# Performance work log

Hardware: AMD Instinct MI355X
Metric: run time of the kernel (lower is better)

Reference implementation:

```python
import jax, jax.numpy as jnp
import numpy as np

TEMP = 0.1
W1, W2 = 0.5, 0.5
W3 = 1.0 - W1 - W2  # = 0.0, as in the original module defaults


def setup_inputs() -> dict:
    key = jax.random.key(0)
    ks = jax.random.split(key, 8)
    N, D = 131072, 256
    C1, C2, C3 = 1000, 100, 20
    features = jax.random.normal(ks[0], (N, D), dtype=jnp.float32) * 0.1
    prototypes_1 = jax.random.normal(ks[1], (C1, D), dtype=jnp.float32)
    labels_1 = jax.random.randint(ks[2], (N,), 0, C1)
    prototypes_2 = jax.random.normal(ks[3], (C2, D), dtype=jnp.float32)
    # ensure every coarse class appears (torch.unique == arange(C))
    labels_2 = jax.random.permutation(ks[4], jnp.arange(N) % C2)
    prototypes_3 = jax.random.normal(ks[5], (C3, D), dtype=jnp.float32)
    labels_3 = jax.random.permutation(ks[6], jnp.arange(N) % C3)
    return {
        "features": features,
        "prototypes_1": prototypes_1,
        "labels_1": labels_1,
        "prototypes_2": prototypes_2,
        "labels_2": labels_2,
        "prototypes_3": prototypes_3,
        "labels_3": labels_3,
    }


def _proto_nce(means, protos):
    # means: [C, D], protos: [C, D]; pos_mask(one_hot of unique=arange) is identity
    sim = (means @ protos.T) / TEMP              # [C, C]
    pos = jnp.diagonal(sim)                      # [C]
    return -jnp.mean(pos - jax.nn.logsumexp(sim, axis=1))


def _segment_mean(features, labels, num_segments):
    sums = jax.ops.segment_sum(features, labels, num_segments=num_segments)
    cnt = jax.ops.segment_sum(jnp.ones((labels.shape[0],), features.dtype),
                              labels, num_segments=num_segments)
    return sums / cnt[:, None]


def reference(features, prototypes_1, labels_1, prototypes_2, labels_2,
              prototypes_3, labels_3):
    # fine level: per-sample InfoNCE against fine prototypes
    fine_sim = (features @ prototypes_1.T) / TEMP            # [N, C1]
    fine_pos = jnp.take_along_axis(fine_sim, labels_1[:, None], axis=1)[:, 0]
    fine_loss = -jnp.mean(fine_pos - jax.nn.logsumexp(fine_sim, axis=1))

    # coarse level: per-class feature means (segment mean == masked-mean loop)
    coarse_means = _segment_mean(features, labels_2, prototypes_2.shape[0])
    coarse_loss = _proto_nce(coarse_means, prototypes_2)

    # con-coarse level
    con_means = _segment_mean(features, labels_3, prototypes_3.shape[0])
    con_coarse_loss = _proto_nce(con_means, prototypes_3)

    loss = W1 * fine_loss + W2 * coarse_loss + W3 * con_coarse_loss
    return (loss, fine_loss, coarse_loss, con_coarse_loss)
```

## Files before the change

kernel.cpp:

```cpp
#include <hip/hip_runtime.h>
#include <math.h>

#define WS_POS   0
#define WS_LSE   1
#define WS_ACC2  2
#define WS_ACC3  3
#define WS_S2    256
#define WS_S3    (256+25600)
#define WS_SEG   163840
#define NROWS    144
#define PART_FLOATS (NROWS*256 + 128)
#define PIMG_BYTE_OFF 131072

#define SC2  14.426950408889634f
#define BIAS 48.0f

typedef __attribute__((ext_vector_type(4))) float f32x4;
typedef __attribute__((ext_vector_type(8))) short short8;

static __device__ __forceinline__ unsigned f2bf(float f) {
    union { float f; unsigned u; } x; x.f = f;
    unsigned r = x.u + 0x7FFFu + ((x.u >> 16) & 1u);
    return r >> 16;
}

__global__ void k_zero(float* __restrict__ p, int count) {
    int i = blockIdx.x * 256 + threadIdx.x;
    if (i < count) p[i] = 0.f;
}

__global__ void k_prep(const float* __restrict__ p1, unsigned short* __restrict__ Pimg,
                       int C1) {
    int e = blockIdx.x * 256 + threadIdx.x;
    int r  = e >> 5;
    int k0 = (e & 31) * 8;
    unsigned h[8];
#pragma unroll
    for (int j = 0; j < 8; ++j)
        h[j] = (r < C1) ? f2bf(p1[(size_t)r * 256 + k0 + j]) : 0u;
    uint4 v;
    v.x = h[0] | (h[1] << 16);
    v.y = h[2] | (h[3] << 16);
    v.z = h[4] | (h[5] << 16);
    v.w = h[6] | (h[7] << 16);
    *(uint4*)(Pimg + (size_t)r * 256 + k0) = v;
}

__global__ __launch_bounds__(256, 2) void k_seg(
        const float* __restrict__ feat, const float* __restrict__ p1,
        const int* __restrict__ l1, const int* __restrict__ l2,
        const int* __restrict__ l3, float* __restrict__ ws,
        int partMask, int useAtomic) {
    __shared__ int labs23[512];
    __shared__ int labs1[512];
    __shared__ float psum[4];
    const int tid  = threadIdx.x;
    const int lane = tid & 63;
    const int wv   = tid >> 6;
    const int g    = lane >> 4;
    const int rs   = lane & 15;
    const int chunk = blockIdx.x >> 1, half = blockIdx.x & 1;
    const int base  = chunk * 512;
    const int dimbase = half * 128 + wv * 32;

    for (int j = tid; j < 512; j += 256) {
        labs23[j] = l2[base + j] | (l3[base + j] << 16);
        labs1[j]  = l1[base + j];
    }
    __syncthreads();

    f32x4 acc[9][2];
#pragma unroll
    for (int mt = 0; mt < 9; ++mt)
#pragma unroll
        for (int nt = 0; nt < 2; ++nt) acc[mt][nt] = (f32x4){0.f, 0.f, 0.f, 0.f};

    float fA[16], pA[16], fB[16], pB[16];
    float posacc = 0.f;

#define LOADSTEP(u, F, P) { \
    const int sl0 = (u) * 32 + 8 * g; \
    _Pragma("unroll") \
    for (int j = 0; j < 8; ++j) { \
        const int sl = sl0 + j; \
        const size_t fb = (size_t)(base + sl) * 256 + dimbase + rs; \
        F[j]     = feat[fb]; \
        F[8 + j] = feat[fb + 16]; \
        const size_t pb = (size_t)labs1[sl] * 256 + dimbase + rs; \
        P[j]     = p1[pb]; \
        P[8 + j] = p1[pb + 16]; \
    } }

#define PROCSTEP(u, F, P) { \
    _Pragma("unroll") \
    for (int j = 0; j < 16; ++j) posacc = fmaf(F[j], P[j], posacc); \
    union { unsigned w[4]; short8 s; } b0, b1; \
    _Pragma("unroll") \
    for (int q = 0; q < 4; ++q) { \
        asm("v_cvt_pk_bf16_f32 %0, %1, %2" : "=v"(b0.w[q]) : "v"(F[2*q]),   "v"(F[2*q+1])); \
        asm("v_cvt_pk_bf16_f32 %0, %1, %2" : "=v"(b1.w[q]) : "v"(F[8+2*q]), "v"(F[8+2*q+1])); \
    } \
    int d2[8], d3[8]; \
    { const int sl0 = (u) * 32 + 8 * g; \
      _Pragma("unroll") \
      for (int j = 0; j < 8; ++j) { \
          const int v = labs23[sl0 + j]; \
          d2[j] = (v & 0xffff) - rs; \
          d3[j] = (v >> 16) - rs; \
      } } \
    _Pragma("unroll") \
    for (int mt = 0; mt < 7; ++mt) { \
        union { unsigned w[4]; short8 s; } af; \
        _Pragma("unroll") \
        for (int q = 0; q < 4; ++q) { \
            unsigned w = (d2[2*q] == mt*16) ? 0x3F80u : 0u; \
            if (d2[2*q+1] == mt*16) w |= 0x3F800000u; \
            af.w[q] = w; \
        } \
        acc[mt][0] = __builtin_amdgcn_mfma_f32_16x16x32_bf16(af.s, b0.s, acc[mt][0], 0, 0, 0); \
        acc[mt][1] = __builtin_amdgcn_mfma_f32_16x16x32_bf16(af.s, b1.s, acc[mt][1], 0, 0, 0); \
    } \
    _Pragma("unroll") \
    for (int mt = 0; mt < 2; ++mt) { \
        union { unsigned w[4]; short8 s; } af; \
        _Pragma("unroll") \
        for (int q = 0; q < 4; ++q) { \
            unsigned w = (d3[2*q] == mt*16) ? 0x3F80u : 0u; \
            if (d3[2*q+1] == mt*16) w |= 0x3F800000u; \
            af.w[q] = w; \
        } \
        acc[7+mt][0] = __builtin_amdgcn_mfma_f32_16x16x32_bf16(af.s, b0.s, acc[7+mt][0], 0, 0, 0); \
        acc[7+mt][1] = __builtin_amdgcn_mfma_f32_16x16x32_bf16(af.s, b1.s, acc[7+mt][1], 0, 0, 0); \
    } }

    LOADSTEP(0, fA, pA);
#pragma unroll 1
    for (int t = 0; t < 16; t += 2) {
        LOADSTEP(t + 1, fB, pB);
        PROCSTEP(t, fA, pA);
        if (t + 2 < 16) LOADSTEP(t + 2, fA, pA);
        PROCSTEP(t + 1, fB, pB);
    }
#undef LOADSTEP
#undef PROCSTEP

    float* part = ws + WS_SEG +
        (size_t)(useAtomic ? (chunk & partMask) : chunk) * PART_FLOATS;
#pragma unroll
    for (int mt = 0; mt < 9; ++mt)
#pragma unroll
        for (int nt = 0; nt < 2; ++nt)
#pragma unroll
            for (int r = 0; r < 4; ++r) {
                float v = acc[mt][nt][r];
                float* dst = &part[(mt * 16 + 4 * g + r) * 256 + dimbase + nt * 16 + rs];
                if (useAtomic) atomicAdd(dst, v); else *dst = v;
            }

    if (half == 0 && tid < 120) {
        float cnt = 0.f;
        const int isl2 = tid < 100;
        const int cls = isl2 ? tid : tid - 100;
#pragma unroll 8
        for (int j = 0; j < 512; ++j) {
            int v = labs23[j];
            int lab = isl2 ? (v & 0xffff) : (v >> 16);
            cnt += (lab == cls) ? 1.f : 0.f;
        }
        float* dst = &part[NROWS * 256 + tid];
        if (useAtomic) atomicAdd(dst, cnt); else *dst = cnt;
    }

#pragma unroll
    for (int m = 1; m < 64; m <<= 1) posacc += __shfl_xor(posacc, m);
    if (lane == 0) psum[wv] = posacc;
    __syncthreads();
    if (tid == 0) atomicAdd(&ws[WS_POS], psum[0] + psum[1] + psum[2] + psum[3]);
}

__global__ __launch_bounds__(256, 4) void k_div(float* __restrict__ ws, int npart) {
    __shared__ float cred[4];
    const int c = blockIdx.x;
    const int d = threadIdx.x;
    const int prow = (c < 100) ? c : 112 + (c - 100);
    float cv = (d < npart) ? ws[WS_SEG + (size_t)d * PART_FLOATS + NROWS * 256 + c] : 0.f;
#pragma unroll
    for (int m = 1; m < 64; m <<= 1) cv += __shfl_xor(cv, m);
    if ((d & 63) == 0) cred[d >> 6] = cv;
    __syncthreads();
    const float cnt = cred[0] + cred[1] + cred[2] + cred[3];
    float a0=0,a1=0,a2=0,a3=0,a4=0,a5=0,a6=0,a7=0;
    int p = 0;
    for (; p + 8 <= npart; p += 8) {
        const float* b = ws + WS_SEG + (size_t)p * PART_FLOATS + prow * 256 + d;
        a0 += b[0 * (size_t)PART_FLOATS];
        a1 += b[1 * (size_t)PART_FLOATS];
        a2 += b[2 * (size_t)PART_FLOATS];
        a3 += b[3 * (size_t)PART_FLOATS];
        a4 += b[4 * (size_t)PART_FLOATS];
        a5 += b[5 * (size_t)PART_FLOATS];
        a6 += b[6 * (size_t)PART_FLOATS];
        a7 += b[7 * (size_t)PART_FLOATS];
    }
    for (; p < npart; ++p)
        a0 += ws[WS_SEG + (size_t)p * PART_FLOATS + prow * 256 + d];
    const float s = ((a0+a1)+(a2+a3)) + ((a4+a5)+(a6+a7));
    ws[256 + ((c < 100) ? c * 256 : 25600 + (c - 100) * 256) + d] = s / cnt;
}

#define LOADB(dst, ptr, OFF) \
    asm volatile("global_load_dwordx4 %0, %1, off offset:" #OFF \
                 : "=v"(dst) : "v"(ptr))
#define LOADB8(buf, ptr) \
    LOADB(buf[0], ptr, 0);   LOADB(buf[1], ptr, 64);  \
    LOADB(buf[2], ptr, 128); LOADB(buf[3], ptr, 192); \
    LOADB(buf[4], ptr, 256); LOADB(buf[5], ptr, 320); \
    LOADB(buf[6], ptr, 384); LOADB(buf[7], ptr, 448)

__global__ __launch_bounds__(256, 2) void k_fine(
        const float* __restrict__ feat, const unsigned short* __restrict__ Pimg,
        float* __restrict__ ws, int C1) {
    __shared__ __align__(16) unsigned short Af[128 * 256];
    __shared__ float Sbuf[128];
    __shared__ float redl[2];
    const int tid  = threadIdx.x;
    const int lane = tid & 63;
    const int wv   = tid >> 6;
    const int g    = lane >> 4;
    const int rs   = lane & 15;
    const int row0 = blockIdx.x * 128;

#pragma unroll
    for (int i = 0; i < 16; ++i) {
        int u = tid + i * 256;
        int r = u >> 5, q8 = u & 31;
        const float* src = feat + (size_t)(row0 + r) * 256 + q8 * 8;
        f32x4 v0 = *(const f32x4*)(src);
        f32x4 v1 = *(const f32x4*)(src + 4);
        uint4 pk;
        asm("v_cvt_pk_bf16_f32 %0, %1, %2" : "=v"(pk.x) : "v"(v0[0]), "v"(v0[1]));
        asm("v_cvt_pk_bf16_f32 %0, %1, %2" : "=v"(pk.y) : "v"(v0[2]), "v"(v0[3]));
        asm("v_cvt_pk_bf16_f32 %0, %1, %2" : "=v"(pk.z) : "v"(v1[0]), "v"(v1[1]));
        asm("v_cvt_pk_bf16_f32 %0, %1, %2" : "=v"(pk.w) : "v"(v1[2]), "v"(v1[3]));
        *(uint4*)((char*)Af + r * 512 + ((q8 * 16) ^ ((r & 7) << 4))) = pk;
    }
    if (tid < 128) Sbuf[tid] = 0.f;
    __syncthreads();

    float es[8][4];
#pragma unroll
    for (int a = 0; a < 8; ++a)
#pragma unroll
        for (int b = 0; b < 4; ++b) es[a][b] = 0.f;

#pragma unroll 1
    for (int p = 0; p < 4; ++p) {
        const int colbase = p * 256 + wv * 64;
        const char* pb = (const char*)Pimg + (size_t)(colbase + rs) * 512 + g * 16;
        short8 bfr[4][8];
        LOADB8(bfr[0], pb);
        LOADB8(bfr[1], pb + 8192);
        LOADB8(bfr[2], pb + 16384);
        LOADB8(bfr[3], pb + 24576);
        asm volatile("s_waitcnt vmcnt(0)" ::: "memory");
        __builtin_amdgcn_sched_barrier(0);

#pragma unroll
        for (int rt = 0; rt < 8; ++rt) {
            f32x4 acc0 = (f32x4){0.f, 0.f, 0.f, 0.f};
            f32x4 acc1 = (f32x4){0.f, 0.f, 0.f, 0.f};
            f32x4 acc2 = (f32x4){0.f, 0.f, 0.f, 0.f};
            f32x4 acc3 = (f32x4){0.f, 0.f, 0.f, 0.f};
            const int ar = rt * 16 + rs;
            const char* abase = (const char*)Af + ar * 512;
            const int sw = (ar & 7) << 4;
#pragma unroll
            for (int ks = 0; ks < 8; ++ks) {
                short8 a = *(const short8*)(abase + ((ks * 64 + g * 16) ^ sw));
                acc0 = __builtin_amdgcn_mfma_f32_16x16x32_bf16(a, bfr[0][ks], acc0, 0, 0, 0);
                acc1 = __builtin_amdgcn_mfma_f32_16x16x32_bf16(a, bfr[1][ks], acc1, 0, 0, 0);
                acc2 = __builtin_amdgcn_mfma_f32_16x16x32_bf16(a, bfr[2][ks], acc2, 0, 0, 0);
                acc3 = __builtin_amdgcn_mfma_f32_16x16x32_bf16(a, bfr[3][ks], acc3, 0, 0, 0);
            }
#pragma unroll
            for (int r = 0; r < 4; ++r) {
                float t0 = fmaf(acc0[r], SC2, -BIAS);
                float t1 = fmaf(acc1[r], SC2, -BIAS);
                float t2 = fmaf(acc2[r], SC2, -BIAS);
                float t3 = fmaf(acc3[r], SC2, -BIAS);
                float e0, e1, e2, e3;
                asm("v_exp_f32 %0, %2\n\t"
                    "v_exp_f32 %1, %3\n\t"
                    "s_nop 1"
                    : "=&v"(e0), "=&v"(e1) : "v"(t0), "v"(t1));
                asm("v_exp_f32 %0, %2\n\t"
                    "v_exp_f32 %1, %3\n\t"
                    "s_nop 1"
                    : "=&v"(e2), "=&v"(e3) : "v"(t2), "v"(t3));
                es[rt][r] += (e0 + e1) + (e2 + e3);
            }
        }
    }
#pragma unroll
    for (int rt = 0; rt < 8; ++rt) {
#pragma unroll
        for (int r = 0; r < 4; ++r) {
            float e = es[rt][r];
            e += __shfl_xor(e, 1);
            e += __shfl_xor(e, 2);
            e += __shfl_xor(e, 4);
            e += __shfl_xor(e, 8);
            if (rs == 0) atomicAdd(&Sbuf[rt * 16 + 4 * g + r], e);
        }
    }
    __syncthreads();
    if (tid < 128) {
        float S = Sbuf[tid] - (float)(1024 - C1) * exp2f(-BIAS);
        float lse = (BIAS + log2f(S)) * 0.6931471805599453f;
#pragma unroll
        for (int m = 1; m < 64; m <<= 1) lse += __shfl_xor(lse, m);
        if (lane == 0) redl[tid >> 6] = lse;
    }
    __syncthreads();
    if (tid == 0) atomicAdd(&ws[WS_LSE], redl[0] + redl[1]);
}

__global__ __launch_bounds__(128, 4) void k_nce(
        const float* __restrict__ p2, const float* __restrict__ p3,
        float* __restrict__ ws) {
    __shared__ __align__(16) float mrow[256];
    __shared__ float sim[128];
    __shared__ float red[2];
    const int b = blockIdx.x;
    const float* means; const float* prot; int C, r, accIdx;
    if (b < 100) { means = ws + WS_S2; prot = p2; C = 100; r = b;       accIdx = WS_ACC2; }
    else         { means = ws + WS_S3; prot = p3; C = 20;  r = b - 100; accIdx = WS_ACC3; }
    const int tid = threadIdx.x;
    const int lane = tid & 63;
    mrow[tid]       = means[(size_t)r * 256 + tid];
    mrow[128 + tid] = means[(size_t)r * 256 + 128 + tid];
    __syncthreads();
    if (tid < C) {
        const f32x4* mr = (const f32x4*)mrow;
        const f32x4* pr = (const f32x4*)(prot + (size_t)tid * 256);
        float acc = 0.f;
#pragma unroll 4
        for (int k = 0; k < 64; ++k) {
            f32x4 m = mr[k], qv = pr[k];
            acc += m[0]*qv[0] + m[1]*qv[1] + m[2]*qv[2] + m[3]*qv[3];
        }
        sim[tid] = acc * 10.0f;
    }
    __syncthreads();
    float v = (tid < C) ? sim[tid] : -1e30f;
#pragma unroll
    for (int m = 1; m < 64; m <<= 1) v = fmaxf(v, __shfl_xor(v, m));
    if (lane == 0) red[tid >> 6] = v;
    __syncthreads();
    const float mx = fmaxf(red[0], red[1]);
    float e = (tid < C) ? __expf(sim[tid] - mx) : 0.f;
#pragma unroll
    for (int m = 1; m < 64; m <<= 1) e += __shfl_xor(e, m);
    __syncthreads();
    if (lane == 0) red[tid >> 6] = e;
    __syncthreads();
    if (tid == 0) {
        float lse = mx + logf(red[0] + red[1]);
        atomicAdd(&ws[accIdx], lse - sim[r]);
    }
}

__global__ void k_final(const float* __restrict__ ws, float* __restrict__ out, float Nf) {
    if (threadIdx.x == 0 && blockIdx.x == 0) {
        float fine   = (ws[WS_LSE] - 10.0f * ws[WS_POS]) / Nf;
        float coarse = ws[WS_ACC2] / 100.0f;
        float con    = ws[WS_ACC3] / 20.0f;
        out[0] = 0.5f * fine + 0.5f * coarse + 0.0f * con;
        out[1] = fine;
        out[2] = coarse;
        out[3] = con;
    }
}

extern "C" void kernel_launch(void* const* d_in, const int* in_sizes, int n_in,
                              void* d_out, int out_size, void* d_ws, size_t ws_size,
                              hipStream_t stream) {
    const float* feat = (const float*)d_in[0];
    const float* p1   = (const float*)d_in[1];
    const int*   l1   = (const int*)d_in[2];
    const float* p2   = (const float*)d_in[3];
    const int*   l2   = (const int*)d_in[4];
    const float* p3   = (const float*)d_in[5];
    const int*   l3   = (const int*)d_in[6];
    float* out = (float*)d_out;
    float* ws  = (float*)d_ws;
    const int n  = in_sizes[0] / 256;
    const int c1 = in_sizes[1] / 256;
    unsigned short* Pimg = (unsigned short*)((char*)d_ws + PIMG_BYTE_OFF);

    const int nchunk = n / 512;
    long nfull = ((long)(ws_size / 4) - WS_SEG) / PART_FLOATS;
    int useAtomic, npart;
    if (nfull >= nchunk) { useAtomic = 0; npart = nchunk; }
    else {
        useAtomic = 1;
        npart = 1;
        while (npart * 2 <= (int)nfull && npart < 32) npart <<= 1;
    }

    k_zero <<<1, 256, 0, stream>>>(ws, 256);
    if (useAtomic)
        k_zero <<<(npart * PART_FLOATS + 255) / 256, 256, 0, stream>>>(ws + WS_SEG, npart * PART_FLOATS);
    k_prep <<<128, 256, 0, stream>>>(p1, Pimg, c1);
    k_seg  <<<nchunk * 2, 256, 0, stream>>>(feat, p1, l1, l2, l3, ws, npart - 1, useAtomic);
    k_div  <<<120, 256, 0, stream>>>(ws, npart);
    k_fine <<<n / 128, 256, 0, stream>>>(feat, Pimg, ws, c1);
    k_nce  <<<120, 128, 0, stream>>>(p2, p3, ws);
    k_final<<<1, 64, 0, stream>>>(ws, out, (float)n);
}
```

Baseline: 170.0 us.

## Double-buffer prototype fragment loads in fine GEMM and fold ws zeroing into prep

The fine-level GEMM loop now processes prototype columns in eight half-width passes with two register buffers, prefetching the next pass's B fragments while MFMAs run on the current one. The first B prefetch is issued before the feature tile is converted into LDS, so that global latency overlaps the A staging. This targets the full vmcnt(0) stall the old loop hit before every 256-column pass, at the cost of partial waits and a different register footprint. Separately, zeroing the first 256 workspace floats moves into k_prep, removing one kernel launch.

```diff
diff --git a/kernel.cpp b/kernel.cpp
--- a/kernel.cpp
+++ b/kernel.cpp
@@ -30,7 +30,8 @@
 }
 
 __global__ void k_prep(const float* __restrict__ p1, unsigned short* __restrict__ Pimg,
-                       int C1) {
+                       float* __restrict__ ws, int C1) {
+    if (blockIdx.x == 0) ws[threadIdx.x] = 0.f;
     int e = blockIdx.x * 256 + threadIdx.x;
     int r  = e >> 5;
     int k0 = (e & 31) * 8;
@@ -230,6 +231,11 @@
     const int rs   = lane & 15;
     const int row0 = blockIdx.x * 128;
 
+#define PBP(p) ((const char*)Pimg + (size_t)((p) * 128 + wv * 32 + rs) * 512 + g * 16)
+
+    short8 bA[2][8], bB[2][8];
+    { const char* pb = PBP(0); LOADB8(bA[0], pb); LOADB8(bA[1], pb + 8192); }
+
 #pragma unroll
     for (int i = 0; i < 16; ++i) {
         int u = tid + i * 256;
@@ -253,54 +259,51 @@
 #pragma unroll
         for (int b = 0; b < 4; ++b) es[a][b] = 0.f;
 
+#define PASS(BUF, pp) { \
+    _Pragma("unroll") \
+    for (int rt = 0; rt < 8; ++rt) { \
+        f32x4 acc0 = (f32x4){0.f, 0.f, 0.f, 0.f}; \
+        f32x4 acc1 = (f32x4){0.f, 0.f, 0.f, 0.f}; \
+        const int ar = rt * 16 + rs; \
+        const char* abase = (const char*)Af + ar * 512; \
+        const int sw = (ar & 7) << 4; \
+        _Pragma("unroll") \
+        for (int ks = 0; ks < 8; ++ks) { \
+            short8 a = *(const short8*)(abase + ((ks * 64 + g * 16) ^ sw)); \
+            acc0 = __builtin_amdgcn_mfma_f32_16x16x32_bf16(a, BUF[0][ks], acc0, 0, 0, 0); \
+            acc1 = __builtin_amdgcn_mfma_f32_16x16x32_bf16(a, BUF[1][ks], acc1, 0, 0, 0); \
+        } \
+        _Pragma("unroll") \
+        for (int r = 0; r < 4; ++r) { \
+            float t0 = fmaf(acc0[r], SC2, -BIAS); \
+            float t1 = fmaf(acc1[r], SC2, -BIAS); \
+            float e0, e1; \
+            asm("v_exp_f32 %0, %2\n\t" \
+                "v_exp_f32 %1, %3\n\t" \
+                "s_nop 1" \
+                : "=&v"(e0), "=&v"(e1) : "v"(t0), "v"(t1)); \
+            es[rt][r] += e0 + e1; \
+        } \
+    } }
+
 #pragma unroll 1
-    for (int p = 0; p < 4; ++p) {
-        const int colbase = p * 256 + wv * 64;
-        const char* pb = (const char*)Pimg + (size_t)(colbase + rs) * 512 + g * 16;
-        short8 bfr[4][8];
-        LOADB8(bfr[0], pb);
-        LOADB8(bfr[1], pb + 8192);
-        LOADB8(bfr[2], pb + 16384);
-        LOADB8(bfr[3], pb + 24576);
-        asm volatile("s_waitcnt vmcnt(0)" ::: "memory");
+    for (int p = 0; p < 8; p += 2) {
+        { const char* pb = PBP(p + 1); LOADB8(bB[0], pb); LOADB8(bB[1], pb + 8192); }
+        asm volatile("s_waitcnt vmcnt(16)" ::: "memory");
         __builtin_amdgcn_sched_barrier(0);
-
-#pragma unroll
-        for (int rt = 0; rt < 8; ++rt) {
-            f32x4 acc0 = (f32x4){0.f, 0.f, 0.f, 0.f};
-            f32x4 acc1 = (f32x4){0.f, 0.f, 0.f, 0.f};
-            f32x4 acc2 = (f32x4){0.f, 0.f, 0.f, 0.f};
-            f32x4 acc3 = (f32x4){0.f, 0.f, 0.f, 0.f};
-            const int ar = rt * 16 + rs;
-            const char* abase = (const char*)Af + ar * 512;
-            const int sw = (ar & 7) << 4;
-#pragma unroll
-            for (int ks = 0; ks < 8; ++ks) {
-                short8 a = *(const short8*)(abase + ((ks * 64 + g * 16) ^ sw));
-                acc0 = __builtin_amdgcn_mfma_f32_16x16x32_bf16(a, bfr[0][ks], acc0, 0, 0, 0);
-                acc1 = __builtin_amdgcn_mfma_f32_16x16x32_bf16(a, bfr[1][ks], acc1, 0, 0, 0);
-                acc2 = __builtin_amdgcn_mfma_f32_16x16x32_bf16(a, bfr[2][ks], acc2, 0, 0, 0);
-                acc3 = __builtin_amdgcn_mfma_f32_16x16x32_bf16(a, bfr[3][ks], acc3, 0, 0, 0);
-            }
-#pragma unroll
-            for (int r = 0; r < 4; ++r) {
-                float t0 = fmaf(acc0[r], SC2, -BIAS);
-                float t1 = fmaf(acc1[r], SC2, -BIAS);
-                float t2 = fmaf(acc2[r], SC2, -BIAS);
-                float t3 = fmaf(acc3[r], SC2, -BIAS);
-                float e0, e1, e2, e3;
-                asm("v_exp_f32 %0, %2\n\t"
-                    "v_exp_f32 %1, %3\n\t"
-                    "s_nop 1"
-                    : "=&v"(e0), "=&v"(e1) : "v"(t0), "v"(t1));
-                asm("v_exp_f32 %0, %2\n\t"
-                    "v_exp_f32 %1, %3\n\t"
-                    "s_nop 1"
-                    : "=&v"(e2), "=&v"(e3) : "v"(t2), "v"(t3));
-                es[rt][r] += (e0 + e1) + (e2 + e3);
-            }
+        PASS(bA, p);
+        if (p + 2 < 8) {
+            const char* pb = PBP(p + 2); LOADB8(bA[0], pb); LOADB8(bA[1], pb + 8192);
+            asm volatile("s_waitcnt vmcnt(16)" ::: "memory");
+        } else {
+            asm volatile("s_waitcnt vmcnt(0)" ::: "memory");
         }
-    }
+        __builtin_amdgcn_sched_barrier(0);
+        PASS(bB, p + 1);
+    }
+#undef PASS
+#undef PBP
+
 #pragma unroll
     for (int rt = 0; rt < 8; ++rt) {
 #pragma unroll
@@ -408,10 +411,9 @@
         while (npart * 2 <= (int)nfull && npart < 32) npart <<= 1;
     }
 
-    k_zero <<<1, 256, 0, stream>>>(ws, 256);
     if (useAtomic)
         k_zero <<<(npart * PART_FLOATS + 255) / 256, 256, 0, stream>>>(ws + WS_SEG, npart * PART_FLOATS);
-    k_prep <<<128, 256, 0, stream>>>(p1, Pimg, c1);
+    k_prep <<<128, 256, 0, stream>>>(p1, Pimg, ws, c1);
     k_seg  <<<nchunk * 2, 256, 0, stream>>>(feat, p1, l1, l2, l3, ws, npart - 1, useAtomic);
     k_div  <<<120, 256, 0, stream>>>(ws, npart);
     k_fine <<<n / 128, 256, 0, stream>>>(feat, Pimg, ws, c1);
```

Result: faster. 161.5 us, median of 2 (-5.0%).
